# Performance work log

Measured on AMD Instinct MI355X. Metric: run time of the kernel, lower is better.

The kernel has to match this reference:

```python
import jax, jax.numpy as jnp
import numpy as np

NS = 10000   # servers
ND = 50000   # devices
H = 512      # hidden dim
E = 300000   # edges per relation
L = 4        # total SAGEConv layers (input + 2 hidden + output)


def segment_mean(vals, seg, num_segments):
    # scatter-mean aggregation (PyG 'mean' aggr); empty segments -> 0
    s = jax.ops.segment_sum(vals, seg, num_segments=num_segments)
    cnt = jax.ops.segment_sum(jnp.ones((seg.shape[0], 1), vals.dtype), seg,
                              num_segments=num_segments)
    return s / jnp.maximum(cnt, 1.0)


def setup_inputs() -> dict:
    key = jax.random.key(0)
    ks = jax.random.split(key, 12)
    scale = 0.05
    return {
        "x_servers": jax.random.normal(ks[0], (NS, 64), jnp.float32),
        "x_devices": jax.random.normal(ks[1], (ND, 32), jnp.float32),
        "W_srv": jax.random.normal(ks[2], (64, H), jnp.float32) * scale,
        "b_srv": jnp.zeros((H,), jnp.float32),
        "W_dev": jax.random.normal(ks[3], (32, H), jnp.float32) * scale,
        "b_dev": jnp.zeros((H,), jnp.float32),
        # rel 0: servers->devices (updates devices); rel 1: devices->servers
        "Wl": jax.random.normal(ks[4], (L, 2, H, H), jnp.float32) * scale,
        "bl": jnp.zeros((L, 2, H), jnp.float32),
        "Wr": jax.random.normal(ks[5], (L, 2, H, H), jnp.float32) * scale,
        "e_sd_src": jax.random.randint(ks[6], (E,), 0, NS, jnp.int32),
        "e_sd_dst": jax.random.randint(ks[7], (E,), 0, ND, jnp.int32),
        "e_ds_src": jax.random.randint(ks[8], (E,), 0, ND, jnp.int32),
        "e_ds_dst": jax.random.randint(ks[9], (E,), 0, NS, jnp.int32),
    }


def reference(x_servers, x_devices, W_srv, b_srv, W_dev, b_dev,
              Wl, bl, Wr, e_sd_src, e_sd_dst, e_ds_src, e_ds_dst):
    # per-type input projection (no activation, as in GNN.forward)
    hs = x_servers @ W_srv + b_srv   # [NS, H]
    hd = x_devices @ W_dev + b_dev   # [ND, H]
    for l in range(L):
        # gather source features per edge, scatter-mean to destination
        agg_d = segment_mean(hs[e_sd_src], e_sd_dst, ND)  # servers -> devices
        agg_s = segment_mean(hd[e_ds_src], e_ds_dst, NS)  # devices -> servers
        # SAGEConv: lin_l(agg) + lin_r(x_dst), then relu
        new_d = jax.nn.relu(agg_d @ Wl[l, 0] + bl[l, 0] + hd @ Wr[l, 0])
        new_s = jax.nn.relu(agg_s @ Wl[l, 1] + bl[l, 1] + hs @ Wr[l, 1])
        hs, hd = new_s, new_d
    return (hs, hd)
```

## Files before the change

### kernel.cpp

```cpp
#include <hip/hip_runtime.h>
#include <cstdint>

#define NSRV 10000
#define NDEV 50000
#define HDIM 512
#define NEDGE 300000
#define NLAY 4
#define SCHUNK 2048

typedef unsigned int u32;
typedef unsigned short u16;

typedef __bf16 bf16x8 __attribute__((ext_vector_type(8)));
typedef float f32x4 __attribute__((ext_vector_type(4)));

__device__ __forceinline__ float bflo(u32 u) { return __uint_as_float(u << 16); }
__device__ __forceinline__ float bfhi(u32 u) { return __uint_as_float(u & 0xffff0000u); }
__device__ __forceinline__ float bf2f(u16 v) { return __uint_as_float((u32)v << 16); }
__device__ __forceinline__ u16 f2bf(float f) {
    u32 u = __float_as_uint(f);
    u += 0x7fffu + ((u >> 16) & 1u);
    return (u16)(u >> 16);
}
__device__ __forceinline__ u32 pack2(float a, float b) {
    return (u32)f2bf(a) | ((u32)f2bf(b) << 16);
}

__global__ void cast_bf16(const float* __restrict__ src, u16* __restrict__ dst, int n2) {
    int i = blockIdx.x * 256 + threadIdx.x;
    if (i < n2) {
        float2 v = *(const float2*)(src + 2 * (size_t)i);
        *(u32*)(dst + 2 * (size_t)i) = pack2(v.x, v.y);
    }
}

__global__ void transpose_w(const float* __restrict__ Wl, const float* __restrict__ Wr,
                            u16* __restrict__ WlT, u16* __restrict__ WrT) {
    __shared__ float t[32][33];
    int z = blockIdx.z;
    const float* Wsrc = ((z < 8) ? Wl : Wr) + (size_t)(z & 7) * HDIM * HDIM;
    u16* Wdst = ((z < 8) ? WlT : WrT) + (size_t)(z & 7) * HDIM * HDIM;
    int n0 = blockIdx.x * 32, k0 = blockIdx.y * 32;
    int x = threadIdx.x, y = threadIdx.y;
#pragma unroll
    for (int i = 0; i < 4; ++i)
        t[y + 8 * i][x] = Wsrc[(size_t)(k0 + y + 8 * i) * HDIM + n0 + x];
    __syncthreads();
    if (x < 16) {
#pragma unroll
        for (int i = 0; i < 4; ++i) {
            int n = n0 + y + 8 * i;
            u32 v = pack2(t[2 * x][y + 8 * i], t[2 * x + 1][y + 8 * i]);
            *(u32*)(Wdst + (size_t)n * HDIM + k0 + 2 * x) = v;
        }
    }
}

template <int K>
__global__ void transpose_wp(const float* __restrict__ W, u16* __restrict__ WT) {
    __shared__ float t[32][33];
    int n0 = blockIdx.x * 32, k0 = blockIdx.y * 32;
    int x = threadIdx.x, y = threadIdx.y;
#pragma unroll
    for (int i = 0; i < 4; ++i)
        t[y + 8 * i][x] = W[(size_t)(k0 + y + 8 * i) * HDIM + n0 + x];
    __syncthreads();
    if (x < 16) {
#pragma unroll
        for (int i = 0; i < 4; ++i) {
            int n = n0 + y + 8 * i;
            u32 v = pack2(t[2 * x][y + 8 * i], t[2 * x + 1][y + 8 * i]);
            *(u32*)(WT + (size_t)n * K + k0 + 2 * x) = v;
        }
    }
}

template <int KTOT>
__launch_bounds__(256, 2)
__global__ void proj_gemm(const u16* __restrict__ A, const u16* __restrict__ B,
                          const float* __restrict__ bias, u16* __restrict__ C, int M) {
    constexpr int NKC = KTOT / 8;
    __shared__ __align__(16) u16 As[NKC][128][8];
    __shared__ __align__(16) u16 Bs[NKC][128][8];
    const int tid = threadIdx.x;
    const int lane = tid & 63;
    const int w = tid >> 6;
    const int m0 = blockIdx.x * 128, n0 = blockIdx.y * 128;
    const int wm = w >> 1, wn = w & 1;
    const int g = lane >> 4, r = lane & 15;

    for (int idx = tid; idx < NKC * 128; idx += 256) {
        int row = idx / NKC, kc = idx % NKC;
        int ra = m0 + row; if (ra > M - 1) ra = M - 1;
        *(uint4*)&As[kc][row][0] = *(const uint4*)(A + (size_t)ra * KTOT + kc * 8);
        *(uint4*)&Bs[kc][row][0] = *(const uint4*)(B + (size_t)(n0 + row) * KTOT + kc * 8);
    }
    __syncthreads();

    f32x4 acc[4][4];
#pragma unroll
    for (int i = 0; i < 4; ++i)
#pragma unroll
        for (int j = 0; j < 4; ++j) acc[i][j] = (f32x4){0.f, 0.f, 0.f, 0.f};

#pragma unroll
    for (int t = 0; t < KTOT / 32; ++t) {
        bf16x8 af[4], bfr[4];
#pragma unroll
        for (int i = 0; i < 4; ++i) {
            af[i]  = *(const bf16x8*)&As[t * 4 + g][wm * 64 + i * 16 + r][0];
            bfr[i] = *(const bf16x8*)&Bs[t * 4 + g][wn * 64 + i * 16 + r][0];
        }
#pragma unroll
        for (int i = 0; i < 4; ++i)
#pragma unroll
            for (int j = 0; j < 4; ++j)
                acc[i][j] = __builtin_amdgcn_mfma_f32_16x16x32_bf16(af[i], bfr[j], acc[i][j], 0, 0, 0);
    }
    __syncthreads();

    float bv[4];
#pragma unroll
    for (int j = 0; j < 4; ++j) bv[j] = bias[n0 + wn * 64 + j * 16 + r];

    u16* ep = ((u16*)As) + w * 1024;
    const int rr = lane >> 3;
    const int cc = (lane & 7) * 8;
#pragma unroll
    for (int i = 0; i < 4; ++i) {
#pragma unroll
        for (int j = 0; j < 4; ++j)
#pragma unroll
            for (int q = 0; q < 4; ++q)
                ep[(g * 4 + q) * 64 + j * 16 + r] = f2bf(acc[i][j][q] + bv[j]);
        __syncthreads();
        int row0 = m0 + wm * 64 + i * 16 + rr;
        int row1 = row0 + 8;
        uint4 v0 = *(uint4*)&ep[rr * 64 + cc];
        uint4 v1 = *(uint4*)&ep[(rr + 8) * 64 + cc];
        if (row0 < M) *(uint4*)(C + (size_t)row0 * HDIM + n0 + wn * 64 + cc) = v0;
        if (row1 < M) *(uint4*)(C + (size_t)row1 * HDIM + n0 + wn * 64 + cc) = v1;
        __syncthreads();
    }
}

__global__ void count_k(const int* __restrict__ d_sd, const int* __restrict__ d_ds,
                        int* __restrict__ cd, int* __restrict__ cs) {
    int i = blockIdx.x * 256 + threadIdx.x;
    if (i < NEDGE) atomicAdd(&cd[d_sd[i]], 1);
    else if (i < 2 * NEDGE) atomicAdd(&cs[d_ds[i - NEDGE]], 1);
}

__global__ void scan_a(const int* __restrict__ c, int* __restrict__ o,
                       int* __restrict__ csum, int n) {
    __shared__ int wsum[4];
    int tid = threadIdx.x;
    int base = blockIdx.x * SCHUNK;
    int idx0 = base + tid * 8;
    int v[8];
    int s = 0;
#pragma unroll
    for (int i = 0; i < 8; ++i) {
        int idx = idx0 + i;
        v[i] = (idx < n) ? c[idx] : 0;
        s += v[i];
    }
    int lane = tid & 63, wv = tid >> 6;
    int ss = s;
#pragma unroll
    for (int off = 1; off < 64; off <<= 1) {
        int t = __shfl_up(ss, off);
        if (lane >= off) ss += t;
    }
    if (lane == 63) wsum[wv] = ss;
    __syncthreads();
    int woff = 0;
#pragma unroll
    for (int i = 0; i < 4; ++i)
        if (i < wv) woff += wsum[i];
    int ex = woff + ss - s;
#pragma unroll
    for (int i = 0; i < 8; ++i) {
        int idx = idx0 + i;
        if (idx < n) o[idx] = ex;
        ex += v[i];
    }
    if (tid == 255) csum[blockIdx.x] = woff + ss;
}

__global__ void scan_k(const int* __restrict__ cA, int* __restrict__ oA, int* __restrict__ uA, int nA,
                       const int* __restrict__ cB, int* __restrict__ oB, int* __restrict__ uB, int nB) {
    const int* c; int* o; int* u; int n;
    if (blockIdx.x == 0) { c = cA; o = oA; u = uA; n = nA; }
    else                 { c = cB; o = oB; u = uB; n = nB; }
    int lane = threadIdx.x;
    int carry = 0;
    for (int base = 0; base < n; base += 64) {
        int idx = base + lane;
        int v = (idx < n) ? c[idx] : 0;
        int s = v;
#pragma unroll
        for (int off = 1; off < 64; off <<= 1) {
            int t = __shfl_up(s, off);
            if (lane >= off) s += t;
        }
        if (idx < n) { int ex = carry + s - v; o[idx] = ex; u[idx] = ex; }
        carry += __shfl(s, 63);
    }
}

__global__ void scan_c(int* __restrict__ o, int* __restrict__ cur,
                       const int* __restrict__ csx, int n) {
    int i = blockIdx.x * 256 + threadIdx.x;
    if (i < n) {
        int v = o[i] + csx[i / SCHUNK];
        o[i] = v;
        cur[i] = v;
    }
}

__global__ void fill_k(const int* __restrict__ s_sd, const int* __restrict__ d_sd,
                       int* __restrict__ cur_d, int* __restrict__ srcs_d,
                       const int* __restrict__ s_ds, const int* __restrict__ d_ds,
                       int* __restrict__ cur_s, int* __restrict__ srcs_s) {
    int i = blockIdx.x * 256 + threadIdx.x;
    if (i < NEDGE) {
        int p = atomicAdd(&cur_d[d_sd[i]], 1);
        srcs_d[p] = s_sd[i];
    } else if (i < 2 * NEDGE) {
        int j = i - NEDGE;
        int p = atomicAdd(&cur_s[d_ds[j]], 1);
        srcs_s[p] = s_ds[j];
    }
}

__global__ void aggregate_k(const u16* __restrict__ h, const int* __restrict__ offs,
                            const int* __restrict__ cnt, const int* __restrict__ srcs,
                            u16* __restrict__ agg, int ndst) {
    int wv = threadIdx.x >> 6, lane = threadIdx.x & 63;
    int d = blockIdx.x * 4 + wv;
    if (d >= ndst) return;
    int beg = offs[d], deg = cnt[d];
    float acc[8] = {0.f, 0.f, 0.f, 0.f, 0.f, 0.f, 0.f, 0.f};
    const size_t lanecol = (size_t)lane * 8;
    auto accum = [&](const uint4& q) {
        acc[0] += bflo(q.x); acc[1] += bfhi(q.x);
        acc[2] += bflo(q.y); acc[3] += bfhi(q.y);
        acc[4] += bflo(q.z); acc[5] += bfhi(q.z);
        acc[6] += bflo(q.w); acc[7] += bfhi(q.w);
    };
    for (int t0 = 0; t0 < deg; t0 += 64) {
        int nch = min(64, deg - t0);
        int sv = (t0 + lane < deg) ? srcs[beg + t0 + lane] : 0;
        int j = 0;
        for (; j + 4 <= nch; j += 4) {
            int s0 = __shfl(sv, j);
            int s1 = __shfl(sv, j + 1);
            int s2 = __shfl(sv, j + 2);
            int s3 = __shfl(sv, j + 3);
            uint4 q0 = *(const uint4*)(h + (size_t)s0 * HDIM + lanecol);
            uint4 q1 = *(const uint4*)(h + (size_t)s1 * HDIM + lanecol);
            uint4 q2 = *(const uint4*)(h + (size_t)s2 * HDIM + lanecol);
            uint4 q3 = *(const uint4*)(h + (size_t)s3 * HDIM + lanecol);
            accum(q0); accum(q1); accum(q2); accum(q3);
        }
        for (; j < nch; ++j) {
            int s = __shfl(sv, j);
            const uint4 q = *(const uint4*)(h + (size_t)s * HDIM + lanecol);
            accum(q);
        }
    }
    float sc = 1.f / (float)(deg > 0 ? deg : 1);
    uint4 o;
    o.x = pack2(acc[0] * sc, acc[1] * sc);
    o.y = pack2(acc[2] * sc, acc[3] * sc);
    o.z = pack2(acc[4] * sc, acc[5] * sc);
    o.w = pack2(acc[6] * sc, acc[7] * sc);
    *(uint4*)(agg + (size_t)d * HDIM + lanecol) = o;
}

__launch_bounds__(256, 2)
__global__ void gemm_fused(const u16* __restrict__ A1, const u16* __restrict__ A2,
                           const u16* __restrict__ B1, const u16* __restrict__ B2,
                           const float* __restrict__ bias, u16* __restrict__ C,
                           int M, int MB) {
    const int b = blockIdx.x;
    const int mi = (b >> 5) * 8 + (b & 7);
    const int ni = (b >> 3) & 3;
    if (mi >= MB) return;

    __shared__ __align__(16) u16 As[2][4][128][8];
    __shared__ __align__(16) u16 Bs[2][4][128][8];
    const int tid = threadIdx.x;
    const int lane = tid & 63;
    const int w = tid >> 6;
    const int m0 = mi * 128, n0 = ni * 128;
    const int wm = w >> 1, wn = w & 1;
    const int g = lane >> 4, r = lane & 15;

    const int srow = tid >> 2;
    const int skc  = tid & 3;

    f32x4 acc[4][4];
#pragma unroll
    for (int i = 0; i < 4; ++i)
#pragma unroll
        for (int j = 0; j < 4; ++j) acc[i][j] = (f32x4){0.f, 0.f, 0.f, 0.f};

    uint4 ra0, ra1, rb0, rb1;
    auto gload = [&](int kt) {
        const u16* Ap = (kt < 16) ? A1 : A2;
        const u16* Bp = (kt < 16) ? B1 : B2;
        const int kb = (kt & 15) * 32 + skc * 8;
        int r0 = m0 + srow;      if (r0 > M - 1) r0 = M - 1;
        int r1 = m0 + srow + 64; if (r1 > M - 1) r1 = M - 1;
        ra0 = *(const uint4*)(Ap + (size_t)r0 * HDIM + kb);
        ra1 = *(const uint4*)(Ap + (size_t)r1 * HDIM + kb);
        rb0 = *(const uint4*)(Bp + (size_t)(n0 + srow) * HDIM + kb);
        rb1 = *(const uint4*)(Bp + (size_t)(n0 + srow + 64) * HDIM + kb);
    };
    auto swrite = [&](int buf) {
        *(uint4*)&As[buf][skc][srow][0]      = ra0;
        *(uint4*)&As[buf][skc][srow + 64][0] = ra1;
        *(uint4*)&Bs[buf][skc][srow][0]      = rb0;
        *(uint4*)&Bs[buf][skc][srow + 64][0] = rb1;
    };
    auto compute = [&](int buf) {
        bf16x8 af[4], bfr[4];
#pragma unroll
        for (int i = 0; i < 4; ++i) {
            af[i]  = *(const bf16x8*)&As[buf][g][wm * 64 + i * 16 + r][0];
            bfr[i] = *(const bf16x8*)&Bs[buf][g][wn * 64 + i * 16 + r][0];
        }
#pragma unroll
        for (int i = 0; i < 4; ++i)
#pragma unroll
            for (int j = 0; j < 4; ++j)
                acc[i][j] = __builtin_amdgcn_mfma_f32_16x16x32_bf16(af[i], bfr[j], acc[i][j], 0, 0, 0);
    };

    gload(0);
    swrite(0);
    __syncthreads();
    for (int kt = 0; kt < 32; ++kt) {
        if (kt < 31) gload(kt + 1);
        compute(kt & 1);
        if (kt < 31) swrite((kt + 1) & 1);
        __syncthreads();
    }

    float bv[4];
#pragma unroll
    for (int j = 0; j < 4; ++j) bv[j] = bias[n0 + wn * 64 + j * 16 + r];

    u16* ep = ((u16*)As) + w * 1024;
    const int rr = lane >> 3;
    const int cc = (lane & 7) * 8;
#pragma unroll
    for (int i = 0; i < 4; ++i) {
#pragma unroll
        for (int j = 0; j < 4; ++j)
#pragma unroll
            for (int q = 0; q < 4; ++q)
                ep[(g * 4 + q) * 64 + j * 16 + r] = f2bf(fmaxf(acc[i][j][q] + bv[j], 0.f));
        __syncthreads();
        int row0 = m0 + wm * 64 + i * 16 + rr;
        int row1 = row0 + 8;
        uint4 v0 = *(uint4*)&ep[rr * 64 + cc];
        uint4 v1 = *(uint4*)&ep[(rr + 8) * 64 + cc];
        if (row0 < M) *(uint4*)(C + (size_t)row0 * HDIM + n0 + wn * 64 + cc) = v0;
        if (row1 < M) *(uint4*)(C + (size_t)row1 * HDIM + n0 + wn * 64 + cc) = v1;
        __syncthreads();
    }
}

__global__ void expand_k(float* out, int lo, int hi) {
    const u16* src = (const u16*)out;
    int j = lo + blockIdx.x * 256 + threadIdx.x;
    if (j < hi) {
        float v = bf2f(src[j]);
        out[(size_t)j] = v;
    }
}
__global__ void expand_final(float* out, int n) {
    __shared__ u16 tmp[4096];
    const u16* src = (const u16*)out;
    int tid = threadIdx.x;
    for (int i = tid; i < n; i += blockDim.x) tmp[i] = src[i];
    __syncthreads();
    for (int i = tid; i < n; i += blockDim.x) out[(size_t)i] = bf2f(tmp[i]);
}

extern "C" void kernel_launch(void* const* d_in, const int* in_sizes, int n_in,
                              void* d_out, int out_size, void* d_ws, size_t ws_size,
                              hipStream_t stream) {
    const float* x_s   = (const float*)d_in[0];
    const float* x_d   = (const float*)d_in[1];
    const float* W_srv = (const float*)d_in[2];
    const float* b_srv = (const float*)d_in[3];
    const float* W_dev = (const float*)d_in[4];
    const float* b_dev = (const float*)d_in[5];
    const float* Wl    = (const float*)d_in[6];
    const float* bl    = (const float*)d_in[7];
    const float* Wr    = (const float*)d_in[8];
    const int* e_sd_src = (const int*)d_in[9];
    const int* e_sd_dst = (const int*)d_in[10];
    const int* e_ds_src = (const int*)d_in[11];
    const int* e_ds_dst = (const int*)d_in[12];

    const size_t NTOT = (size_t)(NSRV + NDEV) * HDIM;
    float* fout = (float*)d_out;
    u16* u = (u16*)d_out;
    u16* hA_s = u;
    u16* hA_d = u + (size_t)NSRV * HDIM;
    u16* hB_s = u + NTOT;
    u16* hB_d = u + NTOT + (size_t)NSRV * HDIM;

    char* p = (char*)d_ws;
    auto carve = [&](size_t bytes) -> void* {
        void* ret = (void*)p;
        p += (bytes + 255) & ~(size_t)255;
        return ret;
    };
    int* cnt_d = (int*)carve((size_t)NDEV * 4);
    int* cnt_s = (int*)carve((size_t)NSRV * 4);
    int* off_d = (int*)carve((size_t)NDEV * 4);
    int* off_s = (int*)carve((size_t)NSRV * 4);
    int* cur_d = (int*)carve((size_t)NDEV * 4);
    int* cur_s = (int*)carve((size_t)NSRV * 4);
    int* src_d = (int*)carve((size_t)NEDGE * 4);
    int* src_s = (int*)carve((size_t)NEDGE * 4);
    int* csum_d = (int*)carve(64 * 4);
    int* csum_s = (int*)carve(64 * 4);
    int* csx_d  = (int*)carve(64 * 4);
    int* csx_s  = (int*)carve(64 * 4);
    u16* WlT   = (u16*)carve((size_t)NLAY * 2 * HDIM * HDIM * 2);
    u16* WrT   = (u16*)carve((size_t)NLAY * 2 * HDIM * HDIM * 2);
    u16* agg   = (u16*)carve((size_t)NDEV * HDIM * 2);
    u16* xb_s  = (u16*)carve((size_t)NSRV * 64 * 2);
    u16* xb_d  = (u16*)carve((size_t)NDEV * 32 * 2);
    u16* WTp_s = (u16*)carve((size_t)HDIM * 64 * 2);
    u16* WTp_d = (u16*)carve((size_t)HDIM * 32 * 2);

    hipMemsetAsync(cnt_d, 0, (size_t)NDEV * 4, stream);
    hipMemsetAsync(cnt_s, 0, (size_t)NSRV * 4, stream);

    cast_bf16<<<(NSRV * 64 / 2 + 255) / 256, 256, 0, stream>>>(x_s, xb_s, NSRV * 64 / 2);
    cast_bf16<<<(NDEV * 32 / 2 + 255) / 256, 256, 0, stream>>>(x_d, xb_d, NDEV * 32 / 2);
    transpose_wp<64><<<dim3(16, 2), dim3(32, 8), 0, stream>>>(W_srv, WTp_s);
    transpose_wp<32><<<dim3(16, 1), dim3(32, 8), 0, stream>>>(W_dev, WTp_d);
    transpose_w<<<dim3(16, 16, 16), dim3(32, 8), 0, stream>>>(Wl, Wr, WlT, WrT);

    proj_gemm<64><<<dim3((NSRV + 127) / 128, 4), 256, 0, stream>>>(xb_s, WTp_s, b_srv, hA_s, NSRV);
    proj_gemm<32><<<dim3((NDEV + 127) / 128, 4), 256, 0, stream>>>(xb_d, WTp_d, b_dev, hA_d, NDEV);

    count_k<<<(2 * NEDGE + 255) / 256, 256, 0, stream>>>(e_sd_dst, e_ds_dst, cnt_d, cnt_s);

    const int NCH_D = (NDEV + SCHUNK - 1) / SCHUNK;
    const int NCH_S = (NSRV + SCHUNK - 1) / SCHUNK;
    scan_a<<<NCH_D, 256, 0, stream>>>(cnt_d, off_d, csum_d, NDEV);
    scan_a<<<NCH_S, 256, 0, stream>>>(cnt_s, off_s, csum_s, NSRV);
    scan_k<<<2, 64, 0, stream>>>(csum_d, csx_d, csx_d, NCH_D, csum_s, csx_s, csx_s, NCH_S);
    scan_c<<<(NDEV + 255) / 256, 256, 0, stream>>>(off_d, cur_d, csx_d, NDEV);
    scan_c<<<(NSRV + 255) / 256, 256, 0, stream>>>(off_s, cur_s, csx_s, NSRV);

    fill_k<<<(2 * NEDGE + 255) / 256, 256, 0, stream>>>(e_sd_src, e_sd_dst, cur_d, src_d,
                                                        e_ds_src, e_ds_dst, cur_s, src_s);

    const int MB_D = (NDEV + 127) / 128;
    const int MB_S = (NSRV + 127) / 128;
    const int GRID_D = ((MB_D + 7) / 8) * 32;
    const int GRID_S = ((MB_S + 7) / 8) * 32;

    for (int l = 0; l < NLAY; ++l) {
        const u16* hs_in = (l & 1) ? hB_s : hA_s;
        const u16* hd_in = (l & 1) ? hB_d : hA_d;
        u16* hs_out = (l & 1) ? hA_s : hB_s;
        u16* hd_out = (l & 1) ? hA_d : hB_d;

        const u16* WlT0 = WlT + (size_t)(l * 2 + 0) * HDIM * HDIM;
        const u16* WrT0 = WrT + (size_t)(l * 2 + 0) * HDIM * HDIM;
        const u16* WlT1 = WlT + (size_t)(l * 2 + 1) * HDIM * HDIM;
        const u16* WrT1 = WrT + (size_t)(l * 2 + 1) * HDIM * HDIM;
        const float* bl0 = bl + (size_t)(l * 2 + 0) * HDIM;
        const float* bl1 = bl + (size_t)(l * 2 + 1) * HDIM;

        aggregate_k<<<(NDEV + 3) / 4, 256, 0, stream>>>(hs_in, off_d, cnt_d, src_d, agg, NDEV);
        gemm_fused<<<GRID_D, 256, 0, stream>>>(agg, hd_in, WlT0, WrT0, bl0, hd_out, NDEV, MB_D);
        aggregate_k<<<(NSRV + 3) / 4, 256, 0, stream>>>(hd_in, off_s, cnt_s, src_s, agg, NSRV);
        gemm_fused<<<GRID_S, 256, 0, stream>>>(agg, hs_in, WlT1, WrT1, bl1, hs_out, NSRV, MB_S);
    }

    int hi = (int)NTOT;
    while (hi > 4000 && (hi % 2 == 0)) {
        int lo = hi / 2;
        int nblk = (hi - lo + 255) / 256;
        expand_k<<<nblk, 256, 0, stream>>>(fout, lo, hi);
        hi = lo;
    }
    expand_final<<<1, 512, 0, stream>>>(fout, hi);
}
```

Baseline: 970.9 us.

## Merge per-relation aggregate/GEMM/scan launches and enlarge GEMM tile to 256 rows

Combines the device and server aggregation into one launch and the two SAGE GEMMs into one grid, using separate agg buffers so both relations can run concurrently. The GEMM moves to 512 threads with a 256x128 output tile, halving B reloads per output and changing the epilogue to stage two sub-tiles at a time. Scan kernels are also merged to cut launch count. This trades larger shared memory and register pressure per block for fewer launches and less tail idle time on the small server GEMM.

```diff
diff --git a/kernel.cpp b/kernel.cpp
--- a/kernel.cpp
+++ b/kernel.cpp
@@ -7,6 +7,8 @@
 #define NEDGE 300000
 #define NLAY 4
 #define SCHUNK 2048
+#define NCH_D ((NDEV + SCHUNK - 1) / SCHUNK)
+#define NCH_S ((NSRV + SCHUNK - 1) / SCHUNK)
 
 typedef unsigned int u32;
 typedef unsigned short u16;
@@ -151,11 +153,15 @@
     else if (i < 2 * NEDGE) atomicAdd(&cs[d_ds[i - NEDGE]], 1);
 }
 
-__global__ void scan_a(const int* __restrict__ c, int* __restrict__ o,
-                       int* __restrict__ csum, int n) {
+__global__ void scan_a_both(const int* __restrict__ cd, int* __restrict__ od, int* __restrict__ csd,
+                            const int* __restrict__ cs, int* __restrict__ os, int* __restrict__ css) {
     __shared__ int wsum[4];
+    int blk = blockIdx.x;
+    const int* c; int* o; int* csum; int n; int cb;
+    if (blk < NCH_D) { c = cd; o = od; csum = csd; n = NDEV; cb = blk; }
+    else             { c = cs; o = os; csum = css; n = NSRV; cb = blk - NCH_D; }
     int tid = threadIdx.x;
-    int base = blockIdx.x * SCHUNK;
+    int base = cb * SCHUNK;
     int idx0 = base + tid * 8;
     int v[8];
     int s = 0;
@@ -185,7 +191,7 @@
         if (idx < n) o[idx] = ex;
         ex += v[i];
     }
-    if (tid == 255) csum[blockIdx.x] = woff + ss;
+    if (tid == 255) csum[cb] = woff + ss;
 }
 
 __global__ void scan_k(const int* __restrict__ cA, int* __restrict__ oA, int* __restrict__ uA, int nA,
@@ -209,13 +215,18 @@
     }
 }
 
-__global__ void scan_c(int* __restrict__ o, int* __restrict__ cur,
-                       const int* __restrict__ csx, int n) {
+__global__ void scan_c_both(int* __restrict__ od, int* __restrict__ curd, const int* __restrict__ csxd,
+                            int* __restrict__ os, int* __restrict__ curs, const int* __restrict__ csxs) {
     int i = blockIdx.x * 256 + threadIdx.x;
-    if (i < n) {
-        int v = o[i] + csx[i / SCHUNK];
-        o[i] = v;
-        cur[i] = v;
+    if (i < NDEV) {
+        int v = od[i] + csxd[i / SCHUNK];
+        od[i] = v;
+        curd[i] = v;
+    } else if (i < NDEV + NSRV) {
+        int j = i - NDEV;
+        int v = os[j] + csxs[j / SCHUNK];
+        os[j] = v;
+        curs[j] = v;
     }
 }
 
@@ -234,13 +245,19 @@
     }
 }
 
-__global__ void aggregate_k(const u16* __restrict__ h, const int* __restrict__ offs,
-                            const int* __restrict__ cnt, const int* __restrict__ srcs,
-                            u16* __restrict__ agg, int ndst) {
+__global__ void aggregate_both(const u16* __restrict__ hs, const u16* __restrict__ hd,
+                               const int* __restrict__ offs_d, const int* __restrict__ cnt_d,
+                               const int* __restrict__ src_d,
+                               const int* __restrict__ offs_s, const int* __restrict__ cnt_s,
+                               const int* __restrict__ src_s,
+                               u16* __restrict__ agg_d, u16* __restrict__ agg_s) {
     int wv = threadIdx.x >> 6, lane = threadIdx.x & 63;
     int d = blockIdx.x * 4 + wv;
-    if (d >= ndst) return;
-    int beg = offs[d], deg = cnt[d];
+    const u16* h; const int* offs; const int* cnt; const int* srcs; u16* agg; int idx;
+    if (d < NDEV)              { h = hs; offs = offs_d; cnt = cnt_d; srcs = src_d; agg = agg_d; idx = d; }
+    else if (d < NDEV + NSRV)  { h = hd; offs = offs_s; cnt = cnt_s; srcs = src_s; agg = agg_s; idx = d - NDEV; }
+    else return;
+    int beg = offs[idx], deg = cnt[idx];
     float acc[8] = {0.f, 0.f, 0.f, 0.f, 0.f, 0.f, 0.f, 0.f};
     const size_t lanecol = (size_t)lane * 8;
     auto accum = [&](const uint4& q) {
@@ -276,25 +293,30 @@
     o.y = pack2(acc[2] * sc, acc[3] * sc);
     o.z = pack2(acc[4] * sc, acc[5] * sc);
     o.w = pack2(acc[6] * sc, acc[7] * sc);
-    *(uint4*)(agg + (size_t)d * HDIM + lanecol) = o;
-}
-
-__launch_bounds__(256, 2)
-__global__ void gemm_fused(const u16* __restrict__ A1, const u16* __restrict__ A2,
-                           const u16* __restrict__ B1, const u16* __restrict__ B2,
-                           const float* __restrict__ bias, u16* __restrict__ C,
-                           int M, int MB) {
-    const int b = blockIdx.x;
+    *(uint4*)(agg + (size_t)idx * HDIM + lanecol) = o;
+}
+
+__launch_bounds__(512, 2)
+__global__ void gemm_both(const u16* __restrict__ A1d, const u16* __restrict__ A2d,
+                          const u16* __restrict__ B1d, const u16* __restrict__ B2d,
+                          const float* __restrict__ bd, u16* __restrict__ Cd, int Md, int MBd, int GD,
+                          const u16* __restrict__ A1s, const u16* __restrict__ A2s,
+                          const u16* __restrict__ B1s, const u16* __restrict__ B2s,
+                          const float* __restrict__ bs, u16* __restrict__ Cs, int Ms, int MBs) {
+    int b = blockIdx.x;
+    const u16 *A1, *A2, *B1, *B2; const float* bias; u16* C; int M, MB;
+    if (b < GD) { A1 = A1d; A2 = A2d; B1 = B1d; B2 = B2d; bias = bd; C = Cd; M = Md; MB = MBd; }
+    else { b -= GD; A1 = A1s; A2 = A2s; B1 = B1s; B2 = B2s; bias = bs; C = Cs; M = Ms; MB = MBs; }
     const int mi = (b >> 5) * 8 + (b & 7);
     const int ni = (b >> 3) & 3;
     if (mi >= MB) return;
 
-    __shared__ __align__(16) u16 As[2][4][128][8];
+    __shared__ __align__(16) u16 As[2][4][256][8];
     __shared__ __align__(16) u16 Bs[2][4][128][8];
     const int tid = threadIdx.x;
     const int lane = tid & 63;
     const int w = tid >> 6;
-    const int m0 = mi * 128, n0 = ni * 128;
+    const int m0 = mi * 256, n0 = ni * 128;
     const int wm = w >> 1, wn = w & 1;
     const int g = lane >> 4, r = lane & 15;
 
@@ -307,23 +329,21 @@
 #pragma unroll
         for (int j = 0; j < 4; ++j) acc[i][j] = (f32x4){0.f, 0.f, 0.f, 0.f};
 
-    uint4 ra0, ra1, rb0, rb1;
+    uint4 ra0, ra1, rb0;
     auto gload = [&](int kt) {
         const u16* Ap = (kt < 16) ? A1 : A2;
         const u16* Bp = (kt < 16) ? B1 : B2;
         const int kb = (kt & 15) * 32 + skc * 8;
-        int r0 = m0 + srow;      if (r0 > M - 1) r0 = M - 1;
-        int r1 = m0 + srow + 64; if (r1 > M - 1) r1 = M - 1;
+        int r0 = m0 + srow;       if (r0 > M - 1) r0 = M - 1;
+        int r1 = m0 + srow + 128; if (r1 > M - 1) r1 = M - 1;
         ra0 = *(const uint4*)(Ap + (size_t)r0 * HDIM + kb);
         ra1 = *(const uint4*)(Ap + (size_t)r1 * HDIM + kb);
         rb0 = *(const uint4*)(Bp + (size_t)(n0 + srow) * HDIM + kb);
-        rb1 = *(const uint4*)(Bp + (size_t)(n0 + srow + 64) * HDIM + kb);
     };
     auto swrite = [&](int buf) {
-        *(uint4*)&As[buf][skc][srow][0]      = ra0;
-        *(uint4*)&As[buf][skc][srow + 64][0] = ra1;
-        *(uint4*)&Bs[buf][skc][srow][0]      = rb0;
-        *(uint4*)&Bs[buf][skc][srow + 64][0] = rb1;
+        *(uint4*)&As[buf][skc][srow][0]       = ra0;
+        *(uint4*)&As[buf][skc][srow + 128][0] = ra1;
+        *(uint4*)&Bs[buf][skc][srow][0]       = rb0;
     };
     auto compute = [&](int buf) {
         bf16x8 af[4], bfr[4];
@@ -353,23 +373,32 @@
 #pragma unroll
     for (int j = 0; j < 4; ++j) bv[j] = bias[n0 + wn * 64 + j * 16 + r];
 
-    u16* ep = ((u16*)As) + w * 1024;
+    u16* ep = ((u16*)As) + w * 2048;
     const int rr = lane >> 3;
     const int cc = (lane & 7) * 8;
 #pragma unroll
-    for (int i = 0; i < 4; ++i) {
-#pragma unroll
-        for (int j = 0; j < 4; ++j)
-#pragma unroll
-            for (int q = 0; q < 4; ++q)
-                ep[(g * 4 + q) * 64 + j * 16 + r] = f2bf(fmaxf(acc[i][j][q] + bv[j], 0.f));
+    for (int ih = 0; ih < 2; ++ih) {
+#pragma unroll
+        for (int ii = 0; ii < 2; ++ii) {
+            int i = ih * 2 + ii;
+#pragma unroll
+            for (int j = 0; j < 4; ++j)
+#pragma unroll
+                for (int q = 0; q < 4; ++q)
+                    ep[ii * 1024 + (g * 4 + q) * 64 + j * 16 + r] =
+                        f2bf(fmaxf(acc[i][j][q] + bv[j], 0.f));
+        }
         __syncthreads();
-        int row0 = m0 + wm * 64 + i * 16 + rr;
-        int row1 = row0 + 8;
-        uint4 v0 = *(uint4*)&ep[rr * 64 + cc];
-        uint4 v1 = *(uint4*)&ep[(rr + 8) * 64 + cc];
-        if (row0 < M) *(uint4*)(C + (size_t)row0 * HDIM + n0 + wn * 64 + cc) = v0;
-        if (row1 < M) *(uint4*)(C + (size_t)row1 * HDIM + n0 + wn * 64 + cc) = v1;
+#pragma unroll
+        for (int ii = 0; ii < 2; ++ii) {
+            int i = ih * 2 + ii;
+            int row0 = m0 + wm * 64 + i * 16 + rr;
+            int row1 = row0 + 8;
+            uint4 v0 = *(uint4*)&ep[ii * 1024 + rr * 64 + cc];
+            uint4 v1 = *(uint4*)&ep[ii * 1024 + (rr + 8) * 64 + cc];
+            if (row0 < M) *(uint4*)(C + (size_t)row0 * HDIM + n0 + wn * 64 + cc) = v0;
+            if (row1 < M) *(uint4*)(C + (size_t)row1 * HDIM + n0 + wn * 64 + cc) = v1;
+        }
         __syncthreads();
     }
 }
@@ -436,7 +465,8 @@
     int* csx_s  = (int*)carve(64 * 4);
     u16* WlT   = (u16*)carve((size_t)NLAY * 2 * HDIM * HDIM * 2);
     u16* WrT   = (u16*)carve((size_t)NLAY * 2 * HDIM * HDIM * 2);
-    u16* agg   = (u16*)carve((size_t)NDEV * HDIM * 2);
+    u16* agg_d = (u16*)carve((size_t)NDEV * HDIM * 2);
+    u16* agg_s = (u16*)carve((size_t)NSRV * HDIM * 2);
     u16* xb_s  = (u16*)carve((size_t)NSRV * 64 * 2);
     u16* xb_d  = (u16*)carve((size_t)NDEV * 32 * 2);
     u16* WTp_s = (u16*)carve((size_t)HDIM * 64 * 2);
@@ -455,22 +485,16 @@
     proj_gemm<32><<<dim3((NDEV + 127) / 128, 4), 256, 0, stream>>>(xb_d, WTp_d, b_dev, hA_d, NDEV);
 
     count_k<<<(2 * NEDGE + 255) / 256, 256, 0, stream>>>(e_sd_dst, e_ds_dst, cnt_d, cnt_s);
-
-    const int NCH_D = (NDEV + SCHUNK - 1) / SCHUNK;
-    const int NCH_S = (NSRV + SCHUNK - 1) / SCHUNK;
-    scan_a<<<NCH_D, 256, 0, stream>>>(cnt_d, off_d, csum_d, NDEV);
-    scan_a<<<NCH_S, 256, 0, stream>>>(cnt_s, off_s, csum_s, NSRV);
+    scan_a_both<<<NCH_D + NCH_S, 256, 0, stream>>>(cnt_d, off_d, csum_d, cnt_s, off_s, csum_s);
     scan_k<<<2, 64, 0, stream>>>(csum_d, csx_d, csx_d, NCH_D, csum_s, csx_s, csx_s, NCH_S);
-    scan_c<<<(NDEV + 255) / 256, 256, 0, stream>>>(off_d, cur_d, csx_d, NDEV);
-    scan_c<<<(NSRV + 255) / 256, 256, 0, stream>>>(off_s, cur_s, csx_s, NSRV);
-
+    scan_c_both<<<(NDEV + NSRV + 255) / 256, 256, 0, stream>>>(off_d, cur_d, csx_d, off_s, cur_s, csx_s);
     fill_k<<<(2 * NEDGE + 255) / 256, 256, 0, stream>>>(e_sd_src, e_sd_dst, cur_d, src_d,
                                                         e_ds_src, e_ds_dst, cur_s, src_s);
 
-    const int MB_D = (NDEV + 127) / 128;
-    const int MB_S = (NSRV + 127) / 128;
-    const int GRID_D = ((MB_D + 7) / 8) * 32;
-    const int GRID_S = ((MB_S + 7) / 8) * 32;
+    const int MB_D = (NDEV + 255) / 256;
+    const int MB_S = (NSRV + 255) / 256;
+    const int GD = ((MB_D + 7) / 8) * 32;
+    const int GS = ((MB_S + 7) / 8) * 32;
 
     for (int l = 0; l < NLAY; ++l) {
         const u16* hs_in = (l & 1) ? hB_s : hA_s;
@@ -485,10 +509,11 @@
         const float* bl0 = bl + (size_t)(l * 2 + 0) * HDIM;
         const float* bl1 = bl + (size_t)(l * 2 + 1) * HDIM;
 
-        aggregate_k<<<(NDEV + 3) / 4, 256, 0, stream>>>(hs_in, off_d, cnt_d, src_d, agg, NDEV);
-        gemm_fused<<<GRID_D, 256, 0, stream>>>(agg, hd_in, WlT0, WrT0, bl0, hd_out, NDEV, MB_D);
-        aggregate_k<<<(NSRV + 3) / 4, 256, 0, stream>>>(hd_in, off_s, cnt_s, src_s, agg, NSRV);
-        gemm_fused<<<GRID_S, 256, 0, stream>>>(agg, hs_in, WlT1, WrT1, bl1, hs_out, NSRV, MB_S);
+        aggregate_both<<<(NDEV + NSRV + 3) / 4, 256, 0, stream>>>(
+            hs_in, hd_in, off_d, cnt_d, src_d, off_s, cnt_s, src_s, agg_d, agg_s);
+        gemm_both<<<GD + GS, 512, 0, stream>>>(
+            agg_d, hd_in, WlT0, WrT0, bl0, hd_out, NDEV, MB_D, GD,
+            agg_s, hs_in, WlT1, WrT1, bl1, hs_out, NSRV, MB_S);
     }
 
     int hi = (int)NTOT;
```

Measured after the change: 852.9 us. 12.2% less time.
